# Optimization experiments

Hardware: AMD Instinct MI355X
Metric: run time of the kernel (lower is better)

Reference implementation:

```python
import jax, jax.numpy as jnp
import numpy as np

N_NODES = 81920
N_EDGES = 1310720
NODES_PER_GRAPH = 320
N_GRAPHS = N_NODES // NODES_PER_GRAPH  # 256
IN_DIM = 64
HID = 64
OUT = 64


def setup_inputs() -> dict:
    key = jax.random.key(0)
    ks = jax.random.split(key, 16)
    x = jax.random.normal(ks[0], (N_NODES, IN_DIM), dtype=jnp.float32)
    edge_index = jax.random.randint(ks[1], (2, N_EDGES), 0, N_NODES, dtype=jnp.int32)
    # sorted graph-membership vector: 256 graphs of 320 nodes each
    batch = (jnp.arange(N_NODES, dtype=jnp.int32) // NODES_PER_GRAPH)
    std = 1.0  # module re-inits nn.Linear weights with N(0, 1)
    dims = [(IN_DIM, HID), (HID, HID), (HID, OUT)]
    params = {}
    for i, (di, do) in enumerate(dims):
        params[f"Wl{i}"] = std * jax.random.normal(ks[2 + 3 * i], (di, do), dtype=jnp.float32)
        params[f"bl{i}"] = jnp.zeros((do,), dtype=jnp.float32)
        params[f"Wr{i}"] = std * jax.random.normal(ks[3 + 3 * i], (di, do), dtype=jnp.float32)
    return dict(x=x, edge_index=edge_index, batch=batch, **params)


def _sage_conv(x, src, dst, Wl, bl, Wr):
    # PyG SAGEConv (aggr='mean', root_weight=True):
    #   out = lin_l(mean_{j in N(i)} x_j) + lin_r(x_i)
    msg = x[src]                                              # [E, d] gather
    agg = jax.ops.segment_sum(msg, dst, num_segments=N_NODES)  # [N, d] scatter-add
    cnt = jax.ops.segment_sum(jnp.ones((src.shape[0],), x.dtype), dst,
                              num_segments=N_NODES)
    agg = agg / jnp.maximum(cnt, 1.0)[:, None]                # mean aggregation
    return agg @ Wl + bl + x @ Wr


def reference(x, edge_index, batch, Wl0, bl0, Wr0, Wl1, bl1, Wr1, Wl2, bl2, Wr2):
    src, dst = edge_index[0], edge_index[1]
    layers = [(Wl0, bl0, Wr0), (Wl1, bl1, Wr1), (Wl2, bl2, Wr2)]
    h = x
    for i, (Wl, bl, Wr) in enumerate(layers):
        h = _sage_conv(h, src, dst, Wl, bl, Wr)
        if i < len(layers) - 1:
            h = jax.nn.relu(h)
            # F.dropout is identity in eval mode (training=False)
    # unbatch + take node 0 of every graph: first index where batch == g
    first_idx = jnp.searchsorted(batch, jnp.arange(N_GRAPHS, dtype=batch.dtype))
    return h[first_idx]  # [N_GRAPHS, OUT]
```

## Files before the change

### kernel.cpp

```cpp
#include <hip/hip_runtime.h>

#define N_NODES 81920
#define N_EDGES 1310720
#define NG 256
#define D 64
#define TM 64
#define SA 65
#define SB 33
#define NB 320
#define NBLK 1280
#define BMW 2560
#define HCHUNK 4096
#define CAP0 1280
#define CAP1 256
#define CAP2 64

typedef __attribute__((ext_vector_type(2))) short sbf2;

__device__ __forceinline__ bool tb(const unsigned* bm, int i) {
    return (bm[i >> 5] >> (i & 31)) & 1u;
}
__device__ __forceinline__ unsigned bf16rne(float f) {
    unsigned u = __float_as_uint(f);
    return (u + 0x7fffu + ((u >> 16) & 1u)) >> 16;
}


__global__ __launch_bounds__(256) void init_ws(float4* __restrict__ aggb4,
                                               unsigned* __restrict__ bms,
                                               int* __restrict__ indeg,
                                               int* __restrict__ n01,
                                               int* __restrict__ cur0,
                                               int* __restrict__ cur1,
                                               int* __restrict__ cur2) {
    int t = blockIdx.x * 256 + threadIdx.x;
    float4 z = make_float4(0.f, 0.f, 0.f, 0.f);
    aggb4[t] = z;
    aggb4[t + NBLK * 256] = z;
    if (t < 3 * BMW) bms[t] = 0u;
    if (t < N_NODES) indeg[t] = 0;
    if (t < 2) n01[t] = 0;
    if (t < NBLK) {
        cur0[t] = t * CAP0;
        cur1[t] = t * CAP1;
        cur2[t] = t * CAP2;
    }
}


__global__ void ff_mark(const int* __restrict__ batch, int* __restrict__ fidx,
                        unsigned* __restrict__ bm2, unsigned* __restrict__ bm1,
                        float* __restrict__ aggf) {
    int i = blockIdx.x * 256 + threadIdx.x;
    int b = batch[i];
    if (i == 0 || batch[i - 1] != b) {
        fidx[b] = i;
        unsigned bit = 1u << (i & 31);
        atomicOr(&bm2[i >> 5], bit);
        atomicOr(&bm1[i >> 5], bit);
        float4* r = (float4*)&aggf[i * D];
        #pragma unroll
        for (int j = 0; j < 16; ++j) r[j] = make_float4(0.f, 0.f, 0.f, 0.f);
    }
}

__global__ void mark_srcs_bm(const int* __restrict__ src, const int* __restrict__ dst,
                             const unsigned* __restrict__ bmD, unsigned* __restrict__ bmS,
                             const unsigned* __restrict__ orsrc) {
    if (orsrc && blockIdx.x == 0) {
        for (int w = threadIdx.x; w < BMW; w += 256)
            if (orsrc[w]) atomicOr(&bmS[w], orsrc[w]);
    }
    int e = blockIdx.x * 256 + threadIdx.x;
    if (e < N_EDGES && tb(bmD, dst[e])) {
        int s = src[e];
        atomicOr(&bmS[s >> 5], 1u << (s & 31));
    }
}


__global__ __launch_bounds__(256) void build(const int* __restrict__ src,
                                             const int* __restrict__ dst,
                                             const unsigned* __restrict__ bm0,
                                             const unsigned* __restrict__ bm1,
                                             const unsigned* __restrict__ bm2,
                                             int* __restrict__ cur0,
                                             int* __restrict__ cur1,
                                             int* __restrict__ cur2,
                                             int* __restrict__ esp0,
                                             int* __restrict__ esp1,
                                             int* __restrict__ esp2,
                                             int* __restrict__ indeg,
                                             int* __restrict__ list0,
                                             int* __restrict__ list1,
                                             int* __restrict__ n0,
                                             int* __restrict__ n1) {
    __shared__ int h0[NBLK], h1s[NBLK], h2s[NBLK];
    const int tid = threadIdx.x;
    const int e0  = blockIdx.x * HCHUNK;

    for (int i = tid; i < NBLK; i += 256) { h0[i] = 0; h1s[i] = 0; h2s[i] = 0; }

    {
        int i = blockIdx.x * 256 + tid;
        int lane = tid & 63;
        bool p0 = tb(bm0, i);
        bool p1 = tb(bm1, i);
        unsigned long long b0 = __ballot(p0);
        int lt = __popcll(b0 & ((1ull << lane) - 1));
        int base = 0;
        if (lane == 0 && b0) base = atomicAdd(n0, __popcll(b0));
        base = __shfl(base, 0);
        if (p0) list0[base + lt] = i;
        unsigned long long b1 = __ballot(p1);
        lt = __popcll(b1 & ((1ull << lane) - 1));
        base = 0;
        if (lane == 0 && b1) base = atomicAdd(n1, __popcll(b1));
        base = __shfl(base, 0);
        if (p1) list1[base + lt] = i;
    }
    __syncthreads();

    for (int e = e0 + tid; e < e0 + HCHUNK; e += 256) {
        int d = dst[e];
        if (tb(bm0, d)) {
            int sb = src[e] >> 6;
            atomicAdd(&h0[sb], 1);
            if (tb(bm1, d)) {
                atomicAdd(&h1s[sb], 1);
                if (tb(bm2, d)) atomicAdd(&h2s[sb], 1);
            }
        }
    }
    __syncthreads();

    for (int i = tid; i < NBLK; i += 256) {
        int c = h0[i];  h0[i]  = c ? atomicAdd(&cur0[i], c) : 0;
        c = h1s[i];     h1s[i] = c ? atomicAdd(&cur1[i], c) : 0;
        c = h2s[i];     h2s[i] = c ? atomicAdd(&cur2[i], c) : 0;
    }
    __syncthreads();

    for (int e = e0 + tid; e < e0 + HCHUNK; e += 256) {
        int d = dst[e];
        if (tb(bm0, d)) {
            int s  = src[e];
            int sb = s >> 6;
            int pk = (d << 6) | (s & 63);
            atomicAdd(&indeg[d], 1);
            int pos = atomicAdd(&h0[sb], 1);
            if (pos < sb * CAP0 + CAP0) esp0[pos] = pk;
            if (tb(bm1, d)) {
                pos = atomicAdd(&h1s[sb], 1);
                if (pos < sb * CAP1 + CAP1) esp1[pos] = pk;
                if (tb(bm2, d)) {
                    pos = atomicAdd(&h2s[sb], 1);
                    if (pos < sb * CAP2 + CAP2) esp2[pos] = pk;
                }
            }
        }
    }
}


__global__ __launch_bounds__(256, 8) void sage_push_bf(
    const float* __restrict__ hin, const int* __restrict__ cur,
    const int* __restrict__ esp, unsigned* __restrict__ aggb, int cap)
{
    __shared__ unsigned Rs[TM * SB];

    const int tid  = threadIdx.x;
    const int base = blockIdx.x * TM;
    const int lane = tid & 63;
    const int w    = tid >> 6;
    const int l5   = lane & 31;
    const int hi   = lane >> 5;

    const int e0 = blockIdx.x * cap;
    const int e1 = min(cur[blockIdx.x], e0 + cap);
    if (e0 == e1) return;

    for (int idx = tid; idx < TM * 32; idx += 256) {
        int m = idx >> 5, k = idx & 31;
        float2 v = *(const float2*)&hin[((base + m) << 6) + (k << 1)];
        Rs[m * SB + k] = bf16rne(v.x) | (bf16rne(v.y) << 16);
    }
    __syncthreads();

    const int chunk = ((e1 - e0) + 3) >> 2;
    int e = e0 + w * chunk;
    const int ee = min(e + chunk, e1);

    for (; e + 64 <= ee; e += 64) {
        int pv = esp[e + lane];
        #pragma unroll
        for (int u = 0; u < 32; ++u) {
            int p = __shfl(pv, (u << 1) + hi);
            unsigned v = Rs[(p & 63) * SB + l5];
            __builtin_amdgcn_global_atomic_fadd_v2bf16(
                (sbf2*)&aggb[((p >> 6) << 5) + l5], *(sbf2*)&v);
        }
    }
    for (; e < ee; ++e) {
        int p = esp[e];
        if (!hi) {
            unsigned v = Rs[(p & 63) * SB + l5];
            __builtin_amdgcn_global_atomic_fadd_v2bf16(
                (sbf2*)&aggb[((p >> 6) << 5) + l5], *(sbf2*)&v);
        }
    }
}


__global__ __launch_bounds__(256, 8) void sage_push_f32(
    const float* __restrict__ hin, const int* __restrict__ cur,
    const int* __restrict__ esp, float* __restrict__ agg, int cap)
{
    __shared__ float Rs[TM * SA];

    const int tid  = threadIdx.x;
    const int base = blockIdx.x * TM;
    const int lane = tid & 63;
    const int w    = tid >> 6;

    const int e0 = blockIdx.x * cap;
    const int e1 = min(cur[blockIdx.x], e0 + cap);
    if (e0 == e1) return;

    for (int idx = tid; idx < TM * D; idx += 256) {
        int m = idx >> 6, k = idx & 63;
        Rs[m * SA + k] = hin[(base << 6) + idx];
    }
    __syncthreads();

    const int chunk = ((e1 - e0) + 3) >> 2;
    int e = e0 + w * chunk;
    const int ee = min(e + chunk, e1);

    for (; e < ee; ++e) {
        int p = esp[e];
        atomicAdd(&agg[(p & 0x7fffffc0) + lane], Rs[(p & 63) * SA + lane]);
    }
}


__global__ __launch_bounds__(256, 4) void sage_finish_sel(
    const float* __restrict__ hin, unsigned* __restrict__ aggb,
    const int* __restrict__ indeg, const int* __restrict__ list,
    const int* __restrict__ pcount, float* __restrict__ hout,
    const float* __restrict__ Wl, const float* __restrict__ bl,
    const float* __restrict__ Wr, int relu)
{
    __shared__ float As[TM * SA];
    __shared__ float Xs[TM * SA];
    __shared__ float invs[TM];
    __shared__ int   nid[TM];

    const int cntv = *pcount;
    const int base = blockIdx.x * TM;
    if (base >= cntv) return;

    const int tid = threadIdx.x;
    if (tid < TM) {
        int n = (base + tid < cntv) ? list[base + tid] : -1;
        nid[tid]  = n;
        invs[tid] = (n >= 0) ? 1.0f / (float)max(indeg[n], 1) : 0.f;
    }
    __syncthreads();
    for (int idx = tid; idx < TM * 32; idx += 256) {
        int m = idx >> 5, k2 = idx & 31;
        int n = nid[m];
        if (n >= 0) {
            unsigned v = aggb[(n << 5) + k2];
            As[m * SA + (k2 << 1)]     = __uint_as_float(v << 16) * invs[m];
            As[m * SA + (k2 << 1) + 1] = __uint_as_float(v & 0xffff0000u) * invs[m];
            aggb[(n << 5) + k2] = 0u;
        } else {
            As[m * SA + (k2 << 1)]     = 0.f;
            As[m * SA + (k2 << 1) + 1] = 0.f;
        }
    }
    for (int idx = tid; idx < TM * D; idx += 256) {
        int m = idx >> 6, k = idx & 63;
        int n = nid[m];
        Xs[m * SA + k] = (n >= 0) ? hin[n * D + k] : 0.f;
    }
    __syncthreads();

    const int j0 = (tid & 15) << 2;
    const int m0 = (tid >> 4) << 2;
    float o[4][4];
    float4 b4 = *(const float4*)&bl[j0];
    #pragma unroll
    for (int mi = 0; mi < 4; ++mi) {
        o[mi][0] = b4.x; o[mi][1] = b4.y; o[mi][2] = b4.z; o[mi][3] = b4.w;
    }
    #pragma unroll 8
    for (int k = 0; k < D; ++k) {
        float4 wl = *(const float4*)&Wl[(k << 6) + j0];
        float4 wr = *(const float4*)&Wr[(k << 6) + j0];
        #pragma unroll
        for (int mi = 0; mi < 4; ++mi) {
            float a = As[(m0 + mi) * SA + k];
            float x = Xs[(m0 + mi) * SA + k];
            o[mi][0] += a * wl.x + x * wr.x;
            o[mi][1] += a * wl.y + x * wr.y;
            o[mi][2] += a * wl.z + x * wr.z;
            o[mi][3] += a * wl.w + x * wr.w;
        }
    }
    #pragma unroll
    for (int mi = 0; mi < 4; ++mi) {
        int n = nid[m0 + mi];
        if (n >= 0) {
            float4 r = make_float4(o[mi][0], o[mi][1], o[mi][2], o[mi][3]);
            if (relu) {
                r.x = fmaxf(r.x, 0.f); r.y = fmaxf(r.y, 0.f);
                r.z = fmaxf(r.z, 0.f); r.w = fmaxf(r.w, 0.f);
            }
            *(float4*)&hout[n * D + j0] = r;
        }
    }
}


__global__ __launch_bounds__(256, 3) void final_gemm_sel(
    const float* __restrict__ hin, const float* __restrict__ agg,
    const int* __restrict__ indeg, const int* __restrict__ fidx,
    const float* __restrict__ Wl, const float* __restrict__ bl,
    const float* __restrict__ Wr, float* __restrict__ out)
{
    __shared__ float As[TM * SA];
    __shared__ float Xs[TM * SA];
    __shared__ int   nid[TM];
    __shared__ float invs[TM];

    const int tid  = threadIdx.x;
    const int base = blockIdx.x * TM;

    if (tid < TM) {
        int n = fidx[base + tid];
        nid[tid]  = n;
        invs[tid] = 1.0f / (float)max(indeg[n], 1);
    }
    __syncthreads();
    for (int idx = tid; idx < TM * D; idx += 256) {
        int m = idx >> 6, k = idx & 63;
        int n = nid[m];
        As[m * SA + k] = agg[n * D + k] * invs[m];
        Xs[m * SA + k] = hin[n * D + k];
    }
    __syncthreads();

    const int j0 = (tid & 15) << 2;
    const int m0 = (tid >> 4) << 2;
    float o[4][4];
    float4 b4 = *(const float4*)&bl[j0];
    #pragma unroll
    for (int mi = 0; mi < 4; ++mi) {
        o[mi][0] = b4.x; o[mi][1] = b4.y; o[mi][2] = b4.z; o[mi][3] = b4.w;
    }
    #pragma unroll 8
    for (int k = 0; k < D; ++k) {
        float4 wl = *(const float4*)&Wl[(k << 6) + j0];
        float4 wr = *(const float4*)&Wr[(k << 6) + j0];
        #pragma unroll
        for (int mi = 0; mi < 4; ++mi) {
            float a = As[(m0 + mi) * SA + k];
            float x = Xs[(m0 + mi) * SA + k];
            o[mi][0] += a * wl.x + x * wr.x;
            o[mi][1] += a * wl.y + x * wr.y;
            o[mi][2] += a * wl.z + x * wr.z;
            o[mi][3] += a * wl.w + x * wr.w;
        }
    }
    #pragma unroll
    for (int mi = 0; mi < 4; ++mi) {
        float4 r = make_float4(o[mi][0], o[mi][1], o[mi][2], o[mi][3]);
        *(float4*)&out[(base + m0 + mi) * D + j0] = r;
    }
}


extern "C" void kernel_launch(void* const* d_in, const int* in_sizes, int n_in,
                              void* d_out, int out_size, void* d_ws, size_t ws_size,
                              hipStream_t stream)
{
    const float* x     = (const float*)d_in[0];
    const int*   ei    = (const int*)d_in[1];
    const int*   batch = (const int*)d_in[2];
    const float* Wl0 = (const float*)d_in[3];
    const float* bl0 = (const float*)d_in[4];
    const float* Wr0 = (const float*)d_in[5];
    const float* Wl1 = (const float*)d_in[6];
    const float* bl1 = (const float*)d_in[7];
    const float* Wr1 = (const float*)d_in[8];
    const float* Wl2 = (const float*)d_in[9];
    const float* bl2 = (const float*)d_in[10];
    const float* Wr2 = (const float*)d_in[11];
    float* out = (float*)d_out;

    const int* src = ei;
    const int* dst = ei + N_EDGES;

    char* ws = (char*)d_ws;
    size_t off = 0;
    auto alloc = [&](size_t bytes) -> void* {
        void* p = ws + off;
        off = (off + bytes + 255) & ~(size_t)255;
        return p;
    };
    int*      cur0  = (int*)alloc(NBLK * sizeof(int));
    int*      cur1  = (int*)alloc(NBLK * sizeof(int));
    int*      cur2  = (int*)alloc(NBLK * sizeof(int));
    int*      fidx  = (int*)alloc(NG * sizeof(int));
    int*      list0 = (int*)alloc(N_NODES * sizeof(int));
    int*      list1 = (int*)alloc(N_NODES * sizeof(int));
    int*      esp0  = (int*)alloc((size_t)NBLK * CAP0 * sizeof(int));
    int*      esp1  = (int*)alloc((size_t)NBLK * CAP1 * sizeof(int));
    int*      esp2  = (int*)alloc((size_t)NBLK * CAP2 * sizeof(int));
    unsigned* aggb  = (unsigned*)alloc((size_t)N_NODES * 32 * sizeof(unsigned));
    float*    aggf  = (float*)alloc((size_t)N_NODES * D * sizeof(float));
    float*    h1    = (float*)alloc((size_t)N_NODES * D * sizeof(float));
    float*    h2    = (float*)alloc((size_t)N_NODES * D * sizeof(float));
    unsigned* bms   = (unsigned*)alloc((size_t)3 * BMW * sizeof(unsigned));
    int*      indeg = (int*)alloc(N_NODES * sizeof(int));
    int*      n01   = (int*)alloc(64 * sizeof(int));
    unsigned* bm0 = bms;
    unsigned* bm1 = bms + BMW;
    unsigned* bm2 = bms + 2 * BMW;
    int* n0 = n01;
    int* n1 = n01 + 1;
    (void)ws_size; (void)in_sizes; (void)n_in; (void)out_size;

    const int EB = (N_EDGES + 255) / 256;

    init_ws<<<NBLK, 256, 0, stream>>>((float4*)aggb, bms, indeg, n01, cur0, cur1, cur2);
    ff_mark<<<NB, 256, 0, stream>>>(batch, fidx, bm2, bm1, aggf);
    mark_srcs_bm<<<EB, 256, 0, stream>>>(src, dst, bm2, bm1, (const unsigned*)nullptr);
    mark_srcs_bm<<<EB, 256, 0, stream>>>(src, dst, bm1, bm0, bm1);
    build<<<NB, 256, 0, stream>>>(src, dst, bm0, bm1, bm2, cur0, cur1, cur2,
                                  esp0, esp1, esp2, indeg, list0, list1, n0, n1);

    sage_push_bf   <<<NBLK, 256, 0, stream>>>(x, cur0, esp0, aggb, CAP0);
    sage_finish_sel<<<NBLK, 256, 0, stream>>>(x, aggb, indeg, list0, n0,
                                              h1, Wl0, bl0, Wr0, 1);
    sage_push_bf   <<<NBLK, 256, 0, stream>>>(h1, cur1, esp1, aggb, CAP1);
    sage_finish_sel<<<NBLK, 256, 0, stream>>>(h1, aggb, indeg, list1, n1,
                                              h2, Wl1, bl1, Wr1, 1);
    sage_push_f32  <<<NBLK, 256, 0, stream>>>(h2, cur2, esp2, aggf, CAP2);
    final_gemm_sel <<<NG / TM, 256, 0, stream>>>(h2, aggf, indeg, fidx, Wl2, bl2, Wr2, out);
}
```

Before: 410.4 us.

## Single-pass edge bucketing in build and dense layer-0 finish kernel

The build kernel now reads each edge once. It keeps per-thread shared-histogram ranks for the layer-0 buckets in registers and writes them after a block-level prefix reservation. Layer-1 and layer-2 bucket slots are taken directly with global atomics. The layer-0 finish now processes every node densely with coalesced loads instead of gathering through an active-node list, which also removes list0 construction. The cost is extra GEMM work on inactive nodes and more global atomic contention for the deeper-layer buckets.

```diff
diff --git a/kernel.cpp b/kernel.cpp
--- a/kernel.cpp
+++ b/kernel.cpp
@@ -11,6 +11,7 @@
 #define NBLK 1280
 #define BMW 2560
 #define HCHUNK 4096
+#define EPT 16
 #define CAP0 1280
 #define CAP1 256
 #define CAP2 64
@@ -91,73 +92,69 @@
                                              int* __restrict__ esp1,
                                              int* __restrict__ esp2,
                                              int* __restrict__ indeg,
-                                             int* __restrict__ list0,
                                              int* __restrict__ list1,
-                                             int* __restrict__ n0,
                                              int* __restrict__ n1) {
-    __shared__ int h0[NBLK], h1s[NBLK], h2s[NBLK];
+    __shared__ int h0[NBLK];
+    __shared__ int b0[NBLK];
     const int tid = threadIdx.x;
     const int e0  = blockIdx.x * HCHUNK;
 
-    for (int i = tid; i < NBLK; i += 256) { h0[i] = 0; h1s[i] = 0; h2s[i] = 0; }
+    for (int i = tid; i < NBLK; i += 256) h0[i] = 0;
 
     {
         int i = blockIdx.x * 256 + tid;
         int lane = tid & 63;
-        bool p0 = tb(bm0, i);
         bool p1 = tb(bm1, i);
-        unsigned long long b0 = __ballot(p0);
-        int lt = __popcll(b0 & ((1ull << lane) - 1));
+        unsigned long long b1 = __ballot(p1);
+        int lt = __popcll(b1 & ((1ull << lane) - 1));
         int base = 0;
-        if (lane == 0 && b0) base = atomicAdd(n0, __popcll(b0));
-        base = __shfl(base, 0);
-        if (p0) list0[base + lt] = i;
-        unsigned long long b1 = __ballot(p1);
-        lt = __popcll(b1 & ((1ull << lane) - 1));
-        base = 0;
         if (lane == 0 && b1) base = atomicAdd(n1, __popcll(b1));
         base = __shfl(base, 0);
         if (p1) list1[base + lt] = i;
     }
     __syncthreads();
 
-    for (int e = e0 + tid; e < e0 + HCHUNK; e += 256) {
+    int pk_r[EPT];
+    int sb_r[EPT];
+    int rk_r[EPT];
+
+    #pragma unroll
+    for (int j = 0; j < EPT; ++j) {
+        int e = e0 + j * 256 + tid;
         int d = dst[e];
-        if (tb(bm0, d)) {
-            int sb = src[e] >> 6;
-            atomicAdd(&h0[sb], 1);
-            if (tb(bm1, d)) {
-                atomicAdd(&h1s[sb], 1);
-                if (tb(bm2, d)) atomicAdd(&h2s[sb], 1);
-            }
-        }
-    }
-    __syncthreads();
-
-    for (int i = tid; i < NBLK; i += 256) {
-        int c = h0[i];  h0[i]  = c ? atomicAdd(&cur0[i], c) : 0;
-        c = h1s[i];     h1s[i] = c ? atomicAdd(&cur1[i], c) : 0;
-        c = h2s[i];     h2s[i] = c ? atomicAdd(&cur2[i], c) : 0;
-    }
-    __syncthreads();
-
-    for (int e = e0 + tid; e < e0 + HCHUNK; e += 256) {
-        int d = dst[e];
+        sb_r[j] = -1;
         if (tb(bm0, d)) {
             int s  = src[e];
             int sb = s >> 6;
             int pk = (d << 6) | (s & 63);
+            pk_r[j] = pk;
+            sb_r[j] = sb;
+            rk_r[j] = atomicAdd(&h0[sb], 1);
             atomicAdd(&indeg[d], 1);
-            int pos = atomicAdd(&h0[sb], 1);
-            if (pos < sb * CAP0 + CAP0) esp0[pos] = pk;
             if (tb(bm1, d)) {
-                pos = atomicAdd(&h1s[sb], 1);
-                if (pos < sb * CAP1 + CAP1) esp1[pos] = pk;
+                int p1 = atomicAdd(&cur1[sb], 1);
+                if (p1 < sb * CAP1 + CAP1) esp1[p1] = pk;
                 if (tb(bm2, d)) {
-                    pos = atomicAdd(&h2s[sb], 1);
-                    if (pos < sb * CAP2 + CAP2) esp2[pos] = pk;
+                    int p2 = atomicAdd(&cur2[sb], 1);
+                    if (p2 < sb * CAP2 + CAP2) esp2[p2] = pk;
                 }
             }
+        }
+    }
+    __syncthreads();
+
+    for (int i = tid; i < NBLK; i += 256) {
+        int c = h0[i];
+        b0[i] = c ? atomicAdd(&cur0[i], c) : 0;
+    }
+    __syncthreads();
+
+    #pragma unroll
+    for (int j = 0; j < EPT; ++j) {
+        int sb = sb_r[j];
+        if (sb >= 0) {
+            int pos = b0[sb] + rk_r[j];
+            if (pos < sb * CAP0 + CAP0) esp0[pos] = pk_r[j];
         }
     }
 }
@@ -244,46 +241,35 @@
 }
 
 
-__global__ __launch_bounds__(256, 4) void sage_finish_sel(
+__global__ __launch_bounds__(256, 4) void sage_finish_dense(
     const float* __restrict__ hin, unsigned* __restrict__ aggb,
-    const int* __restrict__ indeg, const int* __restrict__ list,
-    const int* __restrict__ pcount, float* __restrict__ hout,
+    const int* __restrict__ indeg, float* __restrict__ hout,
     const float* __restrict__ Wl, const float* __restrict__ bl,
-    const float* __restrict__ Wr, int relu)
+    const float* __restrict__ Wr)
 {
     __shared__ float As[TM * SA];
     __shared__ float Xs[TM * SA];
     __shared__ float invs[TM];
-    __shared__ int   nid[TM];
-
-    const int cntv = *pcount;
+
+    const int tid  = threadIdx.x;
     const int base = blockIdx.x * TM;
-    if (base >= cntv) return;
-
-    const int tid = threadIdx.x;
-    if (tid < TM) {
-        int n = (base + tid < cntv) ? list[base + tid] : -1;
-        nid[tid]  = n;
-        invs[tid] = (n >= 0) ? 1.0f / (float)max(indeg[n], 1) : 0.f;
-    }
-    __syncthreads();
+
+    if (tid < TM) invs[tid] = 1.0f / (float)max(indeg[base + tid], 1);
     for (int idx = tid; idx < TM * 32; idx += 256) {
         int m = idx >> 5, k2 = idx & 31;
-        int n = nid[m];
-        if (n >= 0) {
-            unsigned v = aggb[(n << 5) + k2];
-            As[m * SA + (k2 << 1)]     = __uint_as_float(v << 16) * invs[m];
-            As[m * SA + (k2 << 1) + 1] = __uint_as_float(v & 0xffff0000u) * invs[m];
-            aggb[(n << 5) + k2] = 0u;
-        } else {
-            As[m * SA + (k2 << 1)]     = 0.f;
-            As[m * SA + (k2 << 1) + 1] = 0.f;
-        }
+        unsigned v = aggb[(base << 5) + idx];
+        As[m * SA + (k2 << 1)]     = __uint_as_float(v << 16);
+        As[m * SA + (k2 << 1) + 1] = __uint_as_float(v & 0xffff0000u);
+        aggb[(base << 5) + idx] = 0u;
     }
     for (int idx = tid; idx < TM * D; idx += 256) {
         int m = idx >> 6, k = idx & 63;
-        int n = nid[m];
-        Xs[m * SA + k] = (n >= 0) ? hin[n * D + k] : 0.f;
+        Xs[m * SA + k] = hin[(base << 6) + idx];
+    }
+    __syncthreads();
+    for (int idx = tid; idx < TM * D; idx += 256) {
+        int m = idx >> 6, k = idx & 63;
+        As[m * SA + k] *= invs[m];
     }
     __syncthreads();
 
@@ -311,13 +297,83 @@
     }
     #pragma unroll
     for (int mi = 0; mi < 4; ++mi) {
+        float4 r = make_float4(fmaxf(o[mi][0], 0.f), fmaxf(o[mi][1], 0.f),
+                               fmaxf(o[mi][2], 0.f), fmaxf(o[mi][3], 0.f));
+        *(float4*)&hout[(base + m0 + mi) * D + j0] = r;
+    }
+}
+
+
+__global__ __launch_bounds__(256, 4) void sage_finish_sel(
+    const float* __restrict__ hin, unsigned* __restrict__ aggb,
+    const int* __restrict__ indeg, const int* __restrict__ list,
+    const int* __restrict__ pcount, float* __restrict__ hout,
+    const float* __restrict__ Wl, const float* __restrict__ bl,
+    const float* __restrict__ Wr)
+{
+    __shared__ float As[TM * SA];
+    __shared__ float Xs[TM * SA];
+    __shared__ float invs[TM];
+    __shared__ int   nid[TM];
+
+    const int cntv = *pcount;
+    const int base = blockIdx.x * TM;
+    if (base >= cntv) return;
+
+    const int tid = threadIdx.x;
+    if (tid < TM) {
+        int n = (base + tid < cntv) ? list[base + tid] : -1;
+        nid[tid]  = n;
+        invs[tid] = (n >= 0) ? 1.0f / (float)max(indeg[n], 1) : 0.f;
+    }
+    __syncthreads();
+    for (int idx = tid; idx < TM * 32; idx += 256) {
+        int m = idx >> 5, k2 = idx & 31;
+        int n = nid[m];
+        if (n >= 0) {
+            unsigned v = aggb[(n << 5) + k2];
+            As[m * SA + (k2 << 1)]     = __uint_as_float(v << 16) * invs[m];
+            As[m * SA + (k2 << 1) + 1] = __uint_as_float(v & 0xffff0000u) * invs[m];
+        } else {
+            As[m * SA + (k2 << 1)]     = 0.f;
+            As[m * SA + (k2 << 1) + 1] = 0.f;
+        }
+    }
+    for (int idx = tid; idx < TM * D; idx += 256) {
+        int m = idx >> 6, k = idx & 63;
+        int n = nid[m];
+        Xs[m * SA + k] = (n >= 0) ? hin[n * D + k] : 0.f;
+    }
+    __syncthreads();
+
+    const int j0 = (tid & 15) << 2;
+    const int m0 = (tid >> 4) << 2;
+    float o[4][4];
+    float4 b4 = *(const float4*)&bl[j0];
+    #pragma unroll
+    for (int mi = 0; mi < 4; ++mi) {
+        o[mi][0] = b4.x; o[mi][1] = b4.y; o[mi][2] = b4.z; o[mi][3] = b4.w;
+    }
+    #pragma unroll 8
+    for (int k = 0; k < D; ++k) {
+        float4 wl = *(const float4*)&Wl[(k << 6) + j0];
+        float4 wr = *(const float4*)&Wr[(k << 6) + j0];
+        #pragma unroll
+        for (int mi = 0; mi < 4; ++mi) {
+            float a = As[(m0 + mi) * SA + k];
+            float x = Xs[(m0 + mi) * SA + k];
+            o[mi][0] += a * wl.x + x * wr.x;
+            o[mi][1] += a * wl.y + x * wr.y;
+            o[mi][2] += a * wl.z + x * wr.z;
+            o[mi][3] += a * wl.w + x * wr.w;
+        }
+    }
+    #pragma unroll
+    for (int mi = 0; mi < 4; ++mi) {
         int n = nid[m0 + mi];
         if (n >= 0) {
-            float4 r = make_float4(o[mi][0], o[mi][1], o[mi][2], o[mi][3]);
-            if (relu) {
-                r.x = fmaxf(r.x, 0.f); r.y = fmaxf(r.y, 0.f);
-                r.z = fmaxf(r.z, 0.f); r.w = fmaxf(r.w, 0.f);
-            }
+            float4 r = make_float4(fmaxf(o[mi][0], 0.f), fmaxf(o[mi][1], 0.f),
+                                   fmaxf(o[mi][2], 0.f), fmaxf(o[mi][3], 0.f));
             *(float4*)&hout[n * D + j0] = r;
         }
     }
@@ -414,7 +470,6 @@
     int*      cur1  = (int*)alloc(NBLK * sizeof(int));
     int*      cur2  = (int*)alloc(NBLK * sizeof(int));
     int*      fidx  = (int*)alloc(NG * sizeof(int));
-    int*      list0 = (int*)alloc(N_NODES * sizeof(int));
     int*      list1 = (int*)alloc(N_NODES * sizeof(int));
     int*      esp0  = (int*)alloc((size_t)NBLK * CAP0 * sizeof(int));
     int*      esp1  = (int*)alloc((size_t)NBLK * CAP1 * sizeof(int));
@@ -429,7 +484,6 @@
     unsigned* bm0 = bms;
     unsigned* bm1 = bms + BMW;
     unsigned* bm2 = bms + 2 * BMW;
-    int* n0 = n01;
     int* n1 = n01 + 1;
     (void)ws_size; (void)in_sizes; (void)n_in; (void)out_size;
 
@@ -440,14 +494,13 @@
     mark_srcs_bm<<<EB, 256, 0, stream>>>(src, dst, bm2, bm1, (const unsigned*)nullptr);
     mark_srcs_bm<<<EB, 256, 0, stream>>>(src, dst, bm1, bm0, bm1);
     build<<<NB, 256, 0, stream>>>(src, dst, bm0, bm1, bm2, cur0, cur1, cur2,
-                                  esp0, esp1, esp2, indeg, list0, list1, n0, n1);
-
-    sage_push_bf   <<<NBLK, 256, 0, stream>>>(x, cur0, esp0, aggb, CAP0);
-    sage_finish_sel<<<NBLK, 256, 0, stream>>>(x, aggb, indeg, list0, n0,
-                                              h1, Wl0, bl0, Wr0, 1);
-    sage_push_bf   <<<NBLK, 256, 0, stream>>>(h1, cur1, esp1, aggb, CAP1);
-    sage_finish_sel<<<NBLK, 256, 0, stream>>>(h1, aggb, indeg, list1, n1,
-                                              h2, Wl1, bl1, Wr1, 1);
-    sage_push_f32  <<<NBLK, 256, 0, stream>>>(h2, cur2, esp2, aggf, CAP2);
-    final_gemm_sel <<<NG / TM, 256, 0, stream>>>(h2, aggf, indeg, fidx, Wl2, bl2, Wr2, out);
-}
+                                  esp0, esp1, esp2, indeg, list1, n1);
+
+    sage_push_bf     <<<NBLK, 256, 0, stream>>>(x, cur0, esp0, aggb, CAP0);
+    sage_finish_dense<<<NBLK, 256, 0, stream>>>(x, aggb, indeg, h1, Wl0, bl0, Wr0);
+    sage_push_bf     <<<NBLK, 256, 0, stream>>>(h1, cur1, esp1, aggb, CAP1);
+    sage_finish_sel  <<<NBLK, 256, 0, stream>>>(h1, aggb, indeg, list1, n1,
+                                                h2, Wl1, bl1, Wr1);
+    sage_push_f32    <<<NBLK, 256, 0, stream>>>(h2, cur2, esp2, aggf, CAP2);
+    final_gemm_sel   <<<NG / TM, 256, 0, stream>>>(h2, aggf, indeg, fidx, Wl2, bl2, Wr2, out);
+}
```

Result: no change. 404.4 us (-1.5%).
